# Kernel optimization log

Hardware: AMD Instinct MI355X
Metric: run time of the kernel (lower is better)

The kernel has to match this reference:

```python
import jax, jax.numpy as jnp
import numpy as np

N_SVC, N_NODE, N_POD = 50000, 20000, 100000
F = 128          # svc/instance/node feature dims (all 128 per init_kwargs)
HID = 128        # hidden_size
OUT = 64         # out_channel
E_SVC, E_PN, E_NP = 1600000, 100000, 100000


def _graph_conv(x, src, dst, n_src, n_dst, W, b):
    """DGL GraphConv with norm='both': D_dst^{-1/2} A D_src^{-1/2} X W + b."""
    ones = jnp.ones(src.shape[0], dtype=x.dtype)
    deg_src = jnp.clip(jax.ops.segment_sum(ones, src, num_segments=n_src), 1.0)
    deg_dst = jnp.clip(jax.ops.segment_sum(ones, dst, num_segments=n_dst), 1.0)
    # normalize at source, gather, scatter-sum to dst, normalize at dst
    h = x * jax.lax.rsqrt(deg_src)[:, None]          # [n_src, F]
    msg = h[src]                                      # [E, F] gather (memory-bound)
    agg = jax.ops.segment_sum(msg, dst, num_segments=n_dst)  # [n_dst, F]
    agg = agg * jax.lax.rsqrt(deg_dst)[:, None]
    return agg @ W + b                                # [n_dst, HID]


def _leaky(h):
    return jnp.where(h > 0, h, 0.01 * h)


def setup_inputs() -> dict:
    key = jax.random.key(0)
    ks = jax.random.split(key, 16)
    d = {
        "x_svc": jax.random.normal(ks[0], (N_SVC, F), jnp.float32),
        "x_pod": jax.random.normal(ks[1], (N_POD, F), jnp.float32),
        "x_node": jax.random.normal(ks[2], (N_NODE, F), jnp.float32),
        "svc_src": jax.random.randint(ks[3], (E_SVC,), 0, N_SVC, jnp.int32),
        "svc_dst": jax.random.randint(ks[4], (E_SVC,), 0, N_SVC, jnp.int32),
        "pod_node_src": jax.random.randint(ks[5], (E_PN,), 0, N_POD, jnp.int32),
        "pod_node_dst": jax.random.randint(ks[6], (E_PN,), 0, N_NODE, jnp.int32),
        "node_pod_src": jax.random.randint(ks[7], (E_NP,), 0, N_NODE, jnp.int32),
        "node_pod_dst": jax.random.randint(ks[8], (E_NP,), 0, N_POD, jnp.int32),
        # GraphConv weights per edge type
        "W_call": jax.random.normal(ks[9], (F, HID), jnp.float32) * (1.0 / np.sqrt(F)),
        "b_call": jnp.zeros((HID,), jnp.float32),
        "W_in": jax.random.normal(ks[10], (F, HID), jnp.float32) * (1.0 / np.sqrt(F)),
        "b_in": jnp.zeros((HID,), jnp.float32),
        "W_ni": jax.random.normal(ks[11], (F, HID), jnp.float32) * (1.0 / np.sqrt(F)),
        "b_ni": jnp.zeros((HID,), jnp.float32),
        # per-node-type output Linear (hidden -> out_channel)
        "W_lin_svc": jax.random.normal(ks[12], (HID, OUT), jnp.float32) * (1.0 / np.sqrt(HID)),
        "b_lin_svc": jnp.zeros((OUT,), jnp.float32),
        "W_lin_node": jax.random.normal(ks[13], (HID, OUT), jnp.float32) * (1.0 / np.sqrt(HID)),
        "b_lin_node": jnp.zeros((OUT,), jnp.float32),
        "W_lin_pod": jax.random.normal(ks[14], (HID, OUT), jnp.float32) * (1.0 / np.sqrt(HID)),
        "b_lin_pod": jnp.zeros((OUT,), jnp.float32),
    }
    return d


def reference(x_svc, x_pod, x_node,
              svc_src, svc_dst, pod_node_src, pod_node_dst,
              node_pod_src, node_pod_dst,
              W_call, b_call, W_in, b_in, W_ni, b_ni,
              W_lin_svc, b_lin_svc, W_lin_node, b_lin_node,
              W_lin_pod, b_lin_pod):
    # HeteroGraphConv (sum aggregate; each dst type receives one edge type here)
    h_svc = _graph_conv(x_svc, svc_src, svc_dst, N_SVC, N_SVC, W_call, b_call)
    h_node = _graph_conv(x_pod, pod_node_src, pod_node_dst, N_POD, N_NODE, W_in, b_in)
    h_pod = _graph_conv(x_node, node_pod_src, node_pod_dst, N_NODE, N_POD, W_ni, b_ni)
    # per-node-type LeakyReLU + Linear
    o_svc = _leaky(h_svc) @ W_lin_svc + b_lin_svc    # [N_SVC, OUT]
    o_node = _leaky(h_node) @ W_lin_node + b_lin_node  # [N_NODE, OUT]
    o_pod = _leaky(h_pod) @ W_lin_pod + b_lin_pod    # [N_POD, OUT]
    return jnp.concatenate([o_svc, o_node, o_pod], axis=0)  # [N_SVC+N_NODE+N_POD, OUT]
```

## Files before the change

kernel.cpp:

```cpp
#include <hip/hip_runtime.h>

typedef __attribute__((ext_vector_type(8))) short short8;
typedef __attribute__((ext_vector_type(4))) float floatx4;

#define N_SVC  50000
#define N_NODE 20000
#define N_POD  100000
#define E_SVC  1600000
#define E_PN   100000
#define E_NP   100000
#define N_TOT  170000
#define E_TOT  1800000
#define NBUCK  1329
#define NBLK   256
#define PER_BLK 7032
#define P_SVC_BASE  0
#define P_NODE_BASE 50048
#define P_POD_BASE  70080
#define P_TOT       170112
#define SVC_WAVES   50048
#define SVC_BLOCKS  12512
#define NP_WAVES    30016
#define NP_BLOCKS   7504

__device__ __forceinline__ unsigned short f2bf(float f) {
  union { float f; unsigned u; } v; v.f = f;
  unsigned r = v.u + 0x7FFFu + ((v.u >> 16) & 1u);
  return (unsigned short)(r >> 16);
}
__device__ __forceinline__ unsigned pack_bf2(float a, float b) {
  return (unsigned)f2bf(a) | ((unsigned)f2bf(b) << 16);
}
__device__ __forceinline__ float bfl(unsigned u) { union { unsigned u; float f; } v; v.u = u << 16; return v.f; }
__device__ __forceinline__ float bfh(unsigned u) { union { unsigned u; float f; } v; v.u = u & 0xFFFF0000u; return v.f; }

__device__ __forceinline__ int dbase_of(int b) {
  if (b <= 391) return b * 6144;
  if (b <= 547) return 2402304 + (b - 391) * 1536;
  return 2641920 + (b - 547) * 512;
}
#define DST_CAP_TOT 3042304
__device__ __forceinline__ int sbase_of(int b) {
  if (b <= 391) return b * 6144;
  if (b <= 1171) return 2402304 + (b - 391) * 512;
  return 2801664 + (b - 1171) * 1536;
}
#define SRC_CAP_TOT 3044352

__device__ __forceinline__ void load_edge(int i,
    const int* __restrict__ svcS, const int* __restrict__ svcD,
    const int* __restrict__ pnS, const int* __restrict__ pnD,
    const int* __restrict__ npS, const int* __restrict__ npD,
    int& S, int& D) {
  if (i < E_SVC)             { S = svcS[i];                         D = svcD[i]; }
  else if (i < E_SVC + E_PN) { int j = i - E_SVC;        S = pnS[j] + 50000;  D = pnD[j] + 50000; }
  else                       { int j = i - E_SVC - E_PN; S = npS[j] + 150000; D = npD[j] + 70000; }
}

__global__ void init_cur(int* __restrict__ dcur, int* __restrict__ scur) {
  int b = blockIdx.x * 1024 + threadIdx.x;
  if (b < NBUCK) { dcur[b] = dbase_of(b); scur[b] = sbase_of(b); }
}

__global__ __launch_bounds__(1024) void scatter_onepass(
    const int* __restrict__ svcS, const int* __restrict__ svcD,
    const int* __restrict__ pnS, const int* __restrict__ pnD,
    const int* __restrict__ npS, const int* __restrict__ npD,
    int* __restrict__ dcur, int* __restrict__ scur,
    unsigned* __restrict__ dstbuf, unsigned char* __restrict__ srcbuf) {
  __shared__ int ldc[NBUCK], lsc[NBUCK];
  const int tid = threadIdx.x;
  for (int t = tid; t < NBUCK; t += 1024) { ldc[t] = 0; lsc[t] = 0; }
  __syncthreads();
  const int lo = blockIdx.x * PER_BLK;
  const int hi = (lo + PER_BLK < E_TOT) ? lo + PER_BLK : E_TOT;
  int Sv[7], Dv[7];
  #pragma unroll
  for (int k = 0; k < 7; ++k) {
    int e = lo + tid + k * 1024;
    if (e < hi) {
      load_edge(e, svcS, svcD, pnS, pnD, npS, npD, Sv[k], Dv[k]);
      atomicAdd(&ldc[Dv[k] >> 7], 1);
      atomicAdd(&lsc[Sv[k] >> 7], 1);
    } else Sv[k] = -1;
  }
  __syncthreads();
  for (int t = tid; t < NBUCK; t += 1024) {
    int c = ldc[t];  ldc[t] = c ? atomicAdd(&dcur[t], c) : 0;
    int c2 = lsc[t]; lsc[t] = c2 ? atomicAdd(&scur[t], c2) : 0;
  }
  __syncthreads();
  #pragma unroll
  for (int k = 0; k < 7; ++k) {
    if (Sv[k] >= 0) {
      int p = atomicAdd(&ldc[Dv[k] >> 7], 1);
      dstbuf[p] = ((unsigned)(Dv[k] & 127) << 18) | (unsigned)Sv[k];
      int q = atomicAdd(&lsc[Sv[k] >> 7], 1);
      srcbuf[q] = (unsigned char)(Sv[k] & 127);
    }
  }
}

__global__ __launch_bounds__(256) void finalize_all(
    const int* __restrict__ dcur, const int* __restrict__ scur,
    const unsigned* __restrict__ dstbuf, const unsigned char* __restrict__ srcbuf,
    int2* __restrict__ rowrange, int* __restrict__ csr, int* __restrict__ cnt_src) {
  __shared__ int lcnt[128], lcur[128];
  __shared__ int s_w0;
  const int tid = threadIdx.x;
  if (blockIdx.x < NBUCK) {
    const int b = blockIdx.x;
    const int base = dbase_of(b);
    const int cnt = dcur[b] - base;
    if (tid < 128) lcnt[tid] = 0;
    __syncthreads();
    for (int e = tid; e < cnt; e += 256) atomicAdd(&lcnt[dstbuf[base + e] >> 18], 1);
    __syncthreads();
    int excl = 0, v = 0;
    if (tid < 128) {
      v = lcnt[tid];
      int lane = tid & 63;
      int x = v;
      #pragma unroll
      for (int off = 1; off < 64; off <<= 1) {
        int y = __shfl_up(x, off, 64);
        if (lane >= off) x += y;
      }
      excl = x - v;
      if (tid == 63) s_w0 = x;
    }
    __syncthreads();
    if (tid < 128) {
      if (tid >= 64) excl += s_w0;
      lcur[tid] = excl;
      int u = b * 128 + tid;
      if (u < N_TOT) rowrange[u] = make_int2(base + excl, base + excl + v);
    }
    __syncthreads();
    for (int e = tid; e < cnt; e += 256) {
      unsigned wv = dstbuf[base + e];
      int p = atomicAdd(&lcur[wv >> 18], 1);
      csr[base + p] = (int)(wv & 0x3FFFFu);
    }
  } else {
    const int b = blockIdx.x - NBUCK;
    const int base = sbase_of(b);
    const int cnt = scur[b] - base;
    if (tid < 128) lcnt[tid] = 0;
    __syncthreads();
    for (int e = tid; e < cnt; e += 256) atomicAdd(&lcnt[srcbuf[base + e]], 1);
    __syncthreads();
    if (tid < 128) {
      int u = b * 128 + tid;
      if (u < N_TOT) cnt_src[u] = lcnt[tid];
    }
  }
}

__global__ void normalize_cast(const float* __restrict__ xs, const float* __restrict__ xp,
                               const float* __restrict__ xn, const int* __restrict__ cs,
                               unsigned* __restrict__ Xn) {
  int i = blockIdx.x * blockDim.x + threadIdx.x;
  if (i >= N_TOT * 32) return;
  int row = i >> 5, c4 = i & 31;
  const float* src;
  if (row < 50000)       src = xs + (size_t)row * 128;
  else if (row < 150000) src = xp + (size_t)(row - 50000) * 128;
  else                   src = xn + (size_t)(row - 150000) * 128;
  int cc = cs[row]; if (cc < 1) cc = 1;
  float r = rsqrtf((float)cc);
  float4 v = ((const float4*)src)[c4];
  uint2 o;
  o.x = pack_bf2(v.x * r, v.y * r);
  o.y = pack_bf2(v.z * r, v.w * r);
  *(uint2*)(Xn + (size_t)row * 64 + c4 * 2) = o;
}

#define ACC8(v) { a0 += bfl(v.x); a1 += bfh(v.x); a2 += bfl(v.y); a3 += bfh(v.y); \
                  a4 += bfl(v.z); a5 += bfh(v.z); a6 += bfl(v.w); a7 += bfh(v.w); }

__global__ __launch_bounds__(256) void aggregate_svc(
    const unsigned* __restrict__ Xn, const int2* __restrict__ rowrange,
    const int* __restrict__ csr, unsigned* __restrict__ aggb) {
  const int lane = threadIdx.x & 63;
  const int gw = blockIdx.x * 4 + (threadIdx.x >> 6);
  const int grp = lane >> 4, l16 = lane & 15;
  const unsigned* Xb = Xn + l16 * 4;
  unsigned* orow = aggb + (size_t)gw * 64 + l16 * 4;
  if (gw >= 50000) {
    if (gw < SVC_WAVES && grp == 0) *(uint4*)orow = (uint4){0u, 0u, 0u, 0u};
    return;
  }
  int2 rr = rowrange[gw];
  int beg = rr.x, end = rr.y;
  int deg = end - beg;
  float a0 = 0.f, a1 = 0.f, a2 = 0.f, a3 = 0.f, a4 = 0.f, a5 = 0.f, a6 = 0.f, a7 = 0.f;
  int e = beg;
  for (; e + 16 <= end; e += 16) {
    int sA = csr[e + grp];
    int sB = csr[e + 4 + grp];
    int sC = csr[e + 8 + grp];
    int sD = csr[e + 12 + grp];
    uint4 vA = *(const uint4*)(Xb + (unsigned)sA * 64);
    uint4 vB = *(const uint4*)(Xb + (unsigned)sB * 64);
    uint4 vC = *(const uint4*)(Xb + (unsigned)sC * 64);
    uint4 vD = *(const uint4*)(Xb + (unsigned)sD * 64);
    ACC8(vA) ACC8(vB) ACC8(vC) ACC8(vD)
  }
  for (; e + 8 <= end; e += 8) {
    int sA = csr[e + grp];
    int sB = csr[e + 4 + grp];
    uint4 vA = *(const uint4*)(Xb + (unsigned)sA * 64);
    uint4 vB = *(const uint4*)(Xb + (unsigned)sB * 64);
    ACC8(vA) ACC8(vB)
  }
  for (; e + 4 <= end; e += 4) {
    int s = csr[e + grp];
    uint4 v = *(const uint4*)(Xb + (unsigned)s * 64);
    ACC8(v)
  }
  if (grp < end - e) {
    int s = csr[e + grp];
    uint4 v = *(const uint4*)(Xb + (unsigned)s * 64);
    ACC8(v)
  }
  a0 += __shfl_xor(a0, 32, 64); a1 += __shfl_xor(a1, 32, 64);
  a2 += __shfl_xor(a2, 32, 64); a3 += __shfl_xor(a3, 32, 64);
  a4 += __shfl_xor(a4, 32, 64); a5 += __shfl_xor(a5, 32, 64);
  a6 += __shfl_xor(a6, 32, 64); a7 += __shfl_xor(a7, 32, 64);
  a0 += __shfl_xor(a0, 16, 64); a1 += __shfl_xor(a1, 16, 64);
  a2 += __shfl_xor(a2, 16, 64); a3 += __shfl_xor(a3, 16, 64);
  a4 += __shfl_xor(a4, 16, 64); a5 += __shfl_xor(a5, 16, 64);
  a6 += __shfl_xor(a6, 16, 64); a7 += __shfl_xor(a7, 16, 64);
  float rd = rsqrtf((float)(deg < 1 ? 1 : deg));
  if (grp == 0) {
    uint4 o;
    o.x = pack_bf2(a0 * rd, a1 * rd);
    o.y = pack_bf2(a2 * rd, a3 * rd);
    o.z = pack_bf2(a4 * rd, a5 * rd);
    o.w = pack_bf2(a6 * rd, a7 * rd);
    *(uint4*)orow = o;
  }
}

__global__ __launch_bounds__(256) void aggregate_np(
    const unsigned* __restrict__ Xn, const int2* __restrict__ rowrange,
    const int* __restrict__ csr, unsigned* __restrict__ aggb) {
  const int lane = threadIdx.x & 63;
  const int w = blockIdx.x * 4 + (threadIdx.x >> 6);
  const int grp = lane >> 4, l16 = lane & 15;
  const unsigned* Xb = Xn + l16 * 4;
  const int row = SVC_WAVES + w * 4 + grp;
  if (row >= P_TOT) return;
  int u; bool valid;
  if (row < P_POD_BASE) { u = row - 48; valid = (row - P_NODE_BASE) < 20000; }
  else                  { u = row - 80; valid = (row - P_POD_BASE) < 100000; }
  unsigned* orow = aggb + (size_t)row * 64 + l16 * 4;
  if (!valid) {
    *(uint4*)orow = (uint4){0u, 0u, 0u, 0u};
    return;
  }
  int2 rr = rowrange[u];
  int beg = rr.x, end = rr.y;
  int deg = end - beg;
  float a0 = 0.f, a1 = 0.f, a2 = 0.f, a3 = 0.f, a4 = 0.f, a5 = 0.f, a6 = 0.f, a7 = 0.f;
  int e = beg;
  for (; e + 2 <= end; e += 2) {
    int s0 = csr[e];
    int s1 = csr[e + 1];
    uint4 v0 = *(const uint4*)(Xb + (unsigned)s0 * 64);
    uint4 v1 = *(const uint4*)(Xb + (unsigned)s1 * 64);
    ACC8(v0) ACC8(v1)
  }
  if (e < end) {
    int s = csr[e];
    uint4 v = *(const uint4*)(Xb + (unsigned)s * 64);
    ACC8(v)
  }
  float rd = rsqrtf((float)(deg < 1 ? 1 : deg));
  uint4 o;
  o.x = pack_bf2(a0 * rd, a1 * rd);
  o.y = pack_bf2(a2 * rd, a3 * rd);
  o.z = pack_bf2(a4 * rd, a5 * rd);
  o.w = pack_bf2(a6 * rd, a7 * rd);
  *(uint4*)orow = o;
}

__global__ void wprep(const float* __restrict__ W0, const float* __restrict__ W1,
                      const float* __restrict__ W2, const float* __restrict__ L0,
                      const float* __restrict__ L1, const float* __restrict__ L2,
                      unsigned short* __restrict__ Wt, unsigned short* __restrict__ Wt2) {
  int i = blockIdx.x * 256 + threadIdx.x;
  if (i < 3 * 16384) {
    int t = i / 16384, r = i % 16384, n = r / 128, k = r % 128;
    const float* W = (t == 0) ? W0 : ((t == 1) ? W1 : W2);
    Wt[i] = f2bf(W[k * 128 + n]);
  } else if (i < 3 * 16384 + 3 * 8192) {
    int j = i - 3 * 16384;
    int t = j / 8192, r = j % 8192, n = r / 128, k = r % 128;
    const float* L = (t == 0) ? L0 : ((t == 1) ? L1 : L2);
    Wt2[j] = f2bf(L[k * 64 + n]);
  }
}

__global__ __launch_bounds__(256) void gemm_fused(
    const unsigned short* __restrict__ aggb,
    const unsigned short* __restrict__ Wt,
    const unsigned short* __restrict__ Wt2,
    const float* __restrict__ b0, const float* __restrict__ b1, const float* __restrict__ b2,
    const float* __restrict__ l0, const float* __restrict__ l1, const float* __restrict__ l2,
    float* __restrict__ out) {
  __shared__ __align__(16) unsigned short sW1[128 * 136];
  __shared__ __align__(16) unsigned short sH[4][16 * 136];
  const int bid = blockIdx.x;
  int t, bl, nb, ntile, padbase, outbase, mcnt;
  if (bid < 226)      { t = 0; bl = bid;       nb = 226; ntile = 782;  padbase = P_SVC_BASE;  outbase = 0;     mcnt = 50000; }
  else if (bid < 316) { t = 1; bl = bid - 226; nb = 90;  ntile = 313;  padbase = P_NODE_BASE; outbase = 50000; mcnt = 20000; }
  else                { t = 2; bl = bid - 316; nb = 452; ntile = 1563; padbase = P_POD_BASE;  outbase = 70000; mcnt = 100000; }
  const float* bp = (t == 0) ? b0 : ((t == 1) ? b1 : b2);
  const float* lp = (t == 0) ? l0 : ((t == 1) ? l1 : l2);

  const unsigned short* W1g = Wt + t * 16384;
  for (int uu = threadIdx.x; uu < 2048; uu += 256) {
    short8 v = *(const short8*)(W1g + uu * 8);
    *(short8*)(&sW1[(uu >> 4) * 136 + (uu & 15) * 8]) = v;
  }
  const int wv = threadIdx.x >> 6, lane = threadIdx.x & 63;
  const int quad = lane >> 4, l16 = lane & 15;

  const unsigned short* W2g = Wt2 + t * 8192;
  short8 w2f[4][4];
  #pragma unroll
  for (int n = 0; n < 4; n++)
    #pragma unroll
    for (int kt = 0; kt < 4; kt++)
      w2f[n][kt] = *(const short8*)(W2g + (n * 16 + l16) * 128 + kt * 32 + quad * 8);
  float bias1[8], bias2[4];
  #pragma unroll
  for (int n = 0; n < 8; n++) bias1[n] = bp[n * 16 + l16];
  #pragma unroll
  for (int n = 0; n < 4; n++) bias2[n] = lp[n * 16 + l16];
  __syncthreads();

  for (int tile = bl; tile < ntile; tile += nb) {
    const unsigned short* Arow = aggb + (size_t)(padbase + tile * 64 + wv * 16 + l16) * 128;
    floatx4 acc[8];
    #pragma unroll
    for (int n = 0; n < 8; n++) acc[n] = (floatx4){0.f, 0.f, 0.f, 0.f};
    #pragma unroll
    for (int kt = 0; kt < 4; kt++) {
      short8 af = *(const short8*)(Arow + kt * 32 + quad * 8);
      #pragma unroll
      for (int n = 0; n < 8; n++) {
        short8 bf = *(const short8*)(&sW1[(n * 16 + l16) * 136 + kt * 32 + quad * 8]);
        acc[n] = __builtin_amdgcn_mfma_f32_16x16x32_bf16(af, bf, acc[n], 0, 0, 0);
      }
    }
    #pragma unroll
    for (int n = 0; n < 8; n++) {
      #pragma unroll
      for (int i = 0; i < 4; i++) {
        float h = acc[n][i] + bias1[n];
        h = (h > 0.f) ? h : 0.01f * h;
        sH[wv][(quad * 4 + i) * 136 + n * 16 + l16] = f2bf(h);
      }
    }
    floatx4 acc2[4];
    #pragma unroll
    for (int n = 0; n < 4; n++) acc2[n] = (floatx4){0.f, 0.f, 0.f, 0.f};
    #pragma unroll
    for (int kt = 0; kt < 4; kt++) {
      short8 af = *(const short8*)(&sH[wv][l16 * 136 + kt * 32 + quad * 8]);
      #pragma unroll
      for (int n = 0; n < 4; n++)
        acc2[n] = __builtin_amdgcn_mfma_f32_16x16x32_bf16(af, w2f[n][kt], acc2[n], 0, 0, 0);
    }
    int r0 = tile * 64 + wv * 16 + quad * 4;
    #pragma unroll
    for (int n = 0; n < 4; n++) {
      #pragma unroll
      for (int i = 0; i < 4; i++) {
        int r = r0 + i;
        if (r < mcnt) out[(size_t)(outbase + r) * 64 + n * 16 + l16] = acc2[n][i] + bias2[n];
      }
    }
  }
}

extern "C" void kernel_launch(void* const* d_in, const int* in_sizes, int n_in,
                              void* d_out, int out_size, void* d_ws, size_t ws_size,
                              hipStream_t stream) {
  const float* x_svc  = (const float*)d_in[0];
  const float* x_pod  = (const float*)d_in[1];
  const float* x_node = (const float*)d_in[2];
  const int* svc_src  = (const int*)d_in[3];
  const int* svc_dst  = (const int*)d_in[4];
  const int* pn_src   = (const int*)d_in[5];
  const int* pn_dst   = (const int*)d_in[6];
  const int* np_src   = (const int*)d_in[7];
  const int* np_dst   = (const int*)d_in[8];
  const float* W_call = (const float*)d_in[9];
  const float* b_call = (const float*)d_in[10];
  const float* W_in   = (const float*)d_in[11];
  const float* b_in   = (const float*)d_in[12];
  const float* W_ni   = (const float*)d_in[13];
  const float* b_ni   = (const float*)d_in[14];
  const float* W_ls   = (const float*)d_in[15];
  const float* b_ls   = (const float*)d_in[16];
  const float* W_ln   = (const float*)d_in[17];
  const float* b_ln   = (const float*)d_in[18];
  const float* W_lp   = (const float*)d_in[19];
  const float* b_lp   = (const float*)d_in[20];
  float* out = (float*)d_out;

  char* ws = (char*)d_ws;
  int*  dcur     = (int*)(ws + 0);
  int*  scur     = (int*)(ws + 5504);
  int2* rowrange = (int2*)(ws + 11008);
  int*  cnt_src  = (int*)(ws + 1371008);
  int*  csr      = (int*)(ws + 2051072);
  unsigned short* Wt  = (unsigned short*)(ws + 14220288);
  unsigned short* Wt2 = (unsigned short*)(ws + 14318592);
  unsigned* Xn     = (unsigned*)(ws + 14367744);
  unsigned* dstbuf = (unsigned*)(ws + 14367744);
  unsigned char* srcbuf = (unsigned char*)(ws + 26537088);
  unsigned* aggb   = (unsigned*)(ws + 57887744);

  init_cur<<<2, 1024, 0, stream>>>(dcur, scur);
  scatter_onepass<<<NBLK, 1024, 0, stream>>>(svc_src, svc_dst, pn_src, pn_dst,
                                             np_src, np_dst, dcur, scur, dstbuf, srcbuf);
  finalize_all<<<2 * NBUCK, 256, 0, stream>>>(dcur, scur, dstbuf, srcbuf,
                                              rowrange, csr, cnt_src);
  wprep<<<288, 256, 0, stream>>>(W_call, W_in, W_ni, W_ls, W_ln, W_lp, Wt, Wt2);
  normalize_cast<<<21250, 256, 0, stream>>>(x_svc, x_pod, x_node, cnt_src, Xn);
  aggregate_svc<<<SVC_BLOCKS, 256, 0, stream>>>(Xn, rowrange, csr, aggb);
  aggregate_np<<<NP_BLOCKS, 256, 0, stream>>>(Xn, rowrange, csr, aggb);
  gemm_fused<<<768, 256, 0, stream>>>((const unsigned short*)aggb, Wt, Wt2,
                                      b_call, b_in, b_ni, b_ls, b_ln, b_lp, out);
}
```

Measured before the change: 313.8 us.

## Fuse pod/node normalization into aggregation, merge init with weight prep, unroll svc gather

Pod and node features are no longer pre-normalized and cast to bf16. The node/pod aggregation now gathers fp32 rows directly and applies the per-source rsqrt degree scaling inline, so the normalize pass only handles service rows. The bucket-cursor init is merged into the weight-prep kernel to save a launch, and the service aggregation gains a 32-edge unrolled loop for more loads in flight. The cost is that the low-degree pod/node gathers read fp32 rows, twice the bytes of bf16, plus an extra cnt_src lookup per edge, and the workspace offsets are reshuffled.

```diff
diff --git a/kernel.cpp b/kernel.cpp
--- a/kernel.cpp
+++ b/kernel.cpp
@@ -57,9 +57,23 @@
   else                       { int j = i - E_SVC - E_PN; S = npS[j] + 150000; D = npD[j] + 70000; }
 }
 
-__global__ void init_cur(int* __restrict__ dcur, int* __restrict__ scur) {
-  int b = blockIdx.x * 1024 + threadIdx.x;
-  if (b < NBUCK) { dcur[b] = dbase_of(b); scur[b] = sbase_of(b); }
+__global__ void wprep_init(const float* __restrict__ W0, const float* __restrict__ W1,
+                           const float* __restrict__ W2, const float* __restrict__ L0,
+                           const float* __restrict__ L1, const float* __restrict__ L2,
+                           unsigned short* __restrict__ Wt, unsigned short* __restrict__ Wt2,
+                           int* __restrict__ dcur, int* __restrict__ scur) {
+  int i = blockIdx.x * 256 + threadIdx.x;
+  if (i < NBUCK) { dcur[i] = dbase_of(i); scur[i] = sbase_of(i); }
+  if (i < 3 * 16384) {
+    int t = i / 16384, r = i % 16384, n = r / 128, k = r % 128;
+    const float* W = (t == 0) ? W0 : ((t == 1) ? W1 : W2);
+    Wt[i] = f2bf(W[k * 128 + n]);
+  } else if (i < 3 * 16384 + 3 * 8192) {
+    int j = i - 3 * 16384;
+    int t = j / 8192, r = j % 8192, n = r / 128, k = r % 128;
+    const float* L = (t == 0) ? L0 : ((t == 1) ? L1 : L2);
+    Wt2[j] = f2bf(L[k * 64 + n]);
+  }
 }
 
 __global__ __launch_bounds__(1024) void scatter_onepass(
@@ -157,16 +171,12 @@
   }
 }
 
-__global__ void normalize_cast(const float* __restrict__ xs, const float* __restrict__ xp,
-                               const float* __restrict__ xn, const int* __restrict__ cs,
+__global__ void normalize_cast(const float* __restrict__ xs, const int* __restrict__ cs,
                                unsigned* __restrict__ Xn) {
   int i = blockIdx.x * blockDim.x + threadIdx.x;
-  if (i >= N_TOT * 32) return;
+  if (i >= N_SVC * 32) return;
   int row = i >> 5, c4 = i & 31;
-  const float* src;
-  if (row < 50000)       src = xs + (size_t)row * 128;
-  else if (row < 150000) src = xp + (size_t)(row - 50000) * 128;
-  else                   src = xn + (size_t)(row - 150000) * 128;
+  const float* src = xs + (size_t)row * 128;
   int cc = cs[row]; if (cc < 1) cc = 1;
   float r = rsqrtf((float)cc);
   float4 v = ((const float4*)src)[c4];
@@ -196,23 +206,42 @@
   int deg = end - beg;
   float a0 = 0.f, a1 = 0.f, a2 = 0.f, a3 = 0.f, a4 = 0.f, a5 = 0.f, a6 = 0.f, a7 = 0.f;
   int e = beg;
+  for (; e + 32 <= end; e += 32) {
+    int s0 = csr[e + grp];
+    int s1 = csr[e + 4 + grp];
+    int s2 = csr[e + 8 + grp];
+    int s3 = csr[e + 12 + grp];
+    int s4 = csr[e + 16 + grp];
+    int s5 = csr[e + 20 + grp];
+    int s6 = csr[e + 24 + grp];
+    int s7 = csr[e + 28 + grp];
+    uint4 v0 = *(const uint4*)(Xb + (unsigned)s0 * 64);
+    uint4 v1 = *(const uint4*)(Xb + (unsigned)s1 * 64);
+    uint4 v2 = *(const uint4*)(Xb + (unsigned)s2 * 64);
+    uint4 v3 = *(const uint4*)(Xb + (unsigned)s3 * 64);
+    uint4 v4 = *(const uint4*)(Xb + (unsigned)s4 * 64);
+    uint4 v5 = *(const uint4*)(Xb + (unsigned)s5 * 64);
+    uint4 v6 = *(const uint4*)(Xb + (unsigned)s6 * 64);
+    uint4 v7 = *(const uint4*)(Xb + (unsigned)s7 * 64);
+    ACC8(v0) ACC8(v1) ACC8(v2) ACC8(v3) ACC8(v4) ACC8(v5) ACC8(v6) ACC8(v7)
+  }
   for (; e + 16 <= end; e += 16) {
-    int sA = csr[e + grp];
-    int sB = csr[e + 4 + grp];
-    int sC = csr[e + 8 + grp];
-    int sD = csr[e + 12 + grp];
-    uint4 vA = *(const uint4*)(Xb + (unsigned)sA * 64);
-    uint4 vB = *(const uint4*)(Xb + (unsigned)sB * 64);
-    uint4 vC = *(const uint4*)(Xb + (unsigned)sC * 64);
-    uint4 vD = *(const uint4*)(Xb + (unsigned)sD * 64);
-    ACC8(vA) ACC8(vB) ACC8(vC) ACC8(vD)
+    int s0 = csr[e + grp];
+    int s1 = csr[e + 4 + grp];
+    int s2 = csr[e + 8 + grp];
+    int s3 = csr[e + 12 + grp];
+    uint4 v0 = *(const uint4*)(Xb + (unsigned)s0 * 64);
+    uint4 v1 = *(const uint4*)(Xb + (unsigned)s1 * 64);
+    uint4 v2 = *(const uint4*)(Xb + (unsigned)s2 * 64);
+    uint4 v3 = *(const uint4*)(Xb + (unsigned)s3 * 64);
+    ACC8(v0) ACC8(v1) ACC8(v2) ACC8(v3)
   }
   for (; e + 8 <= end; e += 8) {
-    int sA = csr[e + grp];
-    int sB = csr[e + 4 + grp];
-    uint4 vA = *(const uint4*)(Xb + (unsigned)sA * 64);
-    uint4 vB = *(const uint4*)(Xb + (unsigned)sB * 64);
-    ACC8(vA) ACC8(vB)
+    int s0 = csr[e + grp];
+    int s1 = csr[e + 4 + grp];
+    uint4 v0 = *(const uint4*)(Xb + (unsigned)s0 * 64);
+    uint4 v1 = *(const uint4*)(Xb + (unsigned)s1 * 64);
+    ACC8(v0) ACC8(v1)
   }
   for (; e + 4 <= end; e += 4) {
     int s = csr[e + grp];
@@ -244,38 +273,53 @@
 }
 
 __global__ __launch_bounds__(256) void aggregate_np(
-    const unsigned* __restrict__ Xn, const int2* __restrict__ rowrange,
+    const float* __restrict__ xp, const float* __restrict__ xn,
+    const int* __restrict__ cnt_src, const int2* __restrict__ rowrange,
     const int* __restrict__ csr, unsigned* __restrict__ aggb) {
   const int lane = threadIdx.x & 63;
   const int w = blockIdx.x * 4 + (threadIdx.x >> 6);
   const int grp = lane >> 4, l16 = lane & 15;
-  const unsigned* Xb = Xn + l16 * 4;
   const int row = SVC_WAVES + w * 4 + grp;
   if (row >= P_TOT) return;
-  int u; bool valid;
-  if (row < P_POD_BASE) { u = row - 48; valid = (row - P_NODE_BASE) < 20000; }
-  else                  { u = row - 80; valid = (row - P_POD_BASE) < 100000; }
+  int u; bool valid; const float* Xf; int soff;
+  if (row < P_POD_BASE) { u = row - 48; valid = (row - P_NODE_BASE) < 20000; Xf = xp; soff = 50000; }
+  else                  { u = row - 80; valid = (row - P_POD_BASE) < 100000; Xf = xn; soff = 150000; }
   unsigned* orow = aggb + (size_t)row * 64 + l16 * 4;
   if (!valid) {
     *(uint4*)orow = (uint4){0u, 0u, 0u, 0u};
     return;
   }
+  const float* Xb = Xf + l16 * 8;
   int2 rr = rowrange[u];
   int beg = rr.x, end = rr.y;
   int deg = end - beg;
   float a0 = 0.f, a1 = 0.f, a2 = 0.f, a3 = 0.f, a4 = 0.f, a5 = 0.f, a6 = 0.f, a7 = 0.f;
   int e = beg;
   for (; e + 2 <= end; e += 2) {
-    int s0 = csr[e];
-    int s1 = csr[e + 1];
-    uint4 v0 = *(const uint4*)(Xb + (unsigned)s0 * 64);
-    uint4 v1 = *(const uint4*)(Xb + (unsigned)s1 * 64);
-    ACC8(v0) ACC8(v1)
+    int s0 = csr[e], s1 = csr[e + 1];
+    int c0 = cnt_src[s0]; if (c0 < 1) c0 = 1;
+    int c1 = cnt_src[s1]; if (c1 < 1) c1 = 1;
+    float r0 = rsqrtf((float)c0), r1 = rsqrtf((float)c1);
+    const float* p0 = Xb + (size_t)(s0 - soff) * 128;
+    const float* p1 = Xb + (size_t)(s1 - soff) * 128;
+    float4 u0 = *(const float4*)p0;
+    float4 u1 = *(const float4*)(p0 + 4);
+    float4 w0 = *(const float4*)p1;
+    float4 w1 = *(const float4*)(p1 + 4);
+    a0 += u0.x * r0 + w0.x * r1; a1 += u0.y * r0 + w0.y * r1;
+    a2 += u0.z * r0 + w0.z * r1; a3 += u0.w * r0 + w0.w * r1;
+    a4 += u1.x * r0 + w1.x * r1; a5 += u1.y * r0 + w1.y * r1;
+    a6 += u1.z * r0 + w1.z * r1; a7 += u1.w * r0 + w1.w * r1;
   }
   if (e < end) {
     int s = csr[e];
-    uint4 v = *(const uint4*)(Xb + (unsigned)s * 64);
-    ACC8(v)
+    int c = cnt_src[s]; if (c < 1) c = 1;
+    float r = rsqrtf((float)c);
+    const float* p = Xb + (size_t)(s - soff) * 128;
+    float4 u0 = *(const float4*)p;
+    float4 u1 = *(const float4*)(p + 4);
+    a0 += u0.x * r; a1 += u0.y * r; a2 += u0.z * r; a3 += u0.w * r;
+    a4 += u1.x * r; a5 += u1.y * r; a6 += u1.z * r; a7 += u1.w * r;
   }
   float rd = rsqrtf((float)(deg < 1 ? 1 : deg));
   uint4 o;
@@ -284,23 +328,6 @@
   o.z = pack_bf2(a4 * rd, a5 * rd);
   o.w = pack_bf2(a6 * rd, a7 * rd);
   *(uint4*)orow = o;
-}
-
-__global__ void wprep(const float* __restrict__ W0, const float* __restrict__ W1,
-                      const float* __restrict__ W2, const float* __restrict__ L0,
-                      const float* __restrict__ L1, const float* __restrict__ L2,
-                      unsigned short* __restrict__ Wt, unsigned short* __restrict__ Wt2) {
-  int i = blockIdx.x * 256 + threadIdx.x;
-  if (i < 3 * 16384) {
-    int t = i / 16384, r = i % 16384, n = r / 128, k = r % 128;
-    const float* W = (t == 0) ? W0 : ((t == 1) ? W1 : W2);
-    Wt[i] = f2bf(W[k * 128 + n]);
-  } else if (i < 3 * 16384 + 3 * 8192) {
-    int j = i - 3 * 16384;
-    int t = j / 8192, r = j % 8192, n = r / 128, k = r % 128;
-    const float* L = (t == 0) ? L0 : ((t == 1) ? L1 : L2);
-    Wt2[j] = f2bf(L[k * 64 + n]);
-  }
 }
 
 __global__ __launch_bounds__(256) void gemm_fused(
@@ -423,18 +450,18 @@
   unsigned short* Wt2 = (unsigned short*)(ws + 14318592);
   unsigned* Xn     = (unsigned*)(ws + 14367744);
   unsigned* dstbuf = (unsigned*)(ws + 14367744);
-  unsigned char* srcbuf = (unsigned char*)(ws + 26537088);
-  unsigned* aggb   = (unsigned*)(ws + 57887744);
-
-  init_cur<<<2, 1024, 0, stream>>>(dcur, scur);
+  unsigned char* srcbuf = (unsigned char*)(ws + 27180032);
+  unsigned* aggb   = (unsigned*)(ws + 30224384);
+
+  wprep_init<<<288, 256, 0, stream>>>(W_call, W_in, W_ni, W_ls, W_ln, W_lp,
+                                      Wt, Wt2, dcur, scur);
   scatter_onepass<<<NBLK, 1024, 0, stream>>>(svc_src, svc_dst, pn_src, pn_dst,
                                              np_src, np_dst, dcur, scur, dstbuf, srcbuf);
   finalize_all<<<2 * NBUCK, 256, 0, stream>>>(dcur, scur, dstbuf, srcbuf,
                                               rowrange, csr, cnt_src);
-  wprep<<<288, 256, 0, stream>>>(W_call, W_in, W_ni, W_ls, W_ln, W_lp, Wt, Wt2);
-  normalize_cast<<<21250, 256, 0, stream>>>(x_svc, x_pod, x_node, cnt_src, Xn);
+  normalize_cast<<<6250, 256, 0, stream>>>(x_svc, cnt_src, Xn);
   aggregate_svc<<<SVC_BLOCKS, 256, 0, stream>>>(Xn, rowrange, csr, aggb);
-  aggregate_np<<<NP_BLOCKS, 256, 0, stream>>>(Xn, rowrange, csr, aggb);
+  aggregate_np<<<NP_BLOCKS, 256, 0, stream>>>(x_pod, x_node, cnt_src, rowrange, csr, aggb);
   gemm_fused<<<768, 256, 0, stream>>>((const unsigned short*)aggb, Wt, Wt2,
                                       b_call, b_in, b_ni, b_ls, b_ln, b_lp, out);
 }
```

New measurement: 303.8 us. -3.2%, faster.
